# Kernel optimization log

Measured on AMD Instinct MI355X. Metric: run time of the kernel, lower is better.

## Reference

```python
import jax, jax.numpy as jnp
import numpy as np

B, T, S0 = 8, 4, 4096
D_MODEL, H, D, R, RANK = 2048, 16, 128, 64, 512
C = D - R  # content dim = 64


def _rope(x, positions):
    # x: [B, H, T, R]; rotate-half style RoPE as in the torch module
    half = x.shape[-1] // 2
    inv_freq = 1.0 / (10000.0 ** (jnp.arange(half, dtype=jnp.float32) / half))
    freqs = positions.astype(jnp.float32)[:, None] * inv_freq[None, :]  # [T, half]
    cos = jnp.cos(freqs)[None, None].astype(x.dtype)
    sin = jnp.sin(freqs)[None, None].astype(x.dtype)
    x1, x2 = x[..., :half], x[..., half:]
    return jnp.concatenate([x1 * cos - x2 * sin, x1 * sin + x2 * cos], axis=-1)


def setup_inputs() -> dict:
    key = jax.random.key(0)
    ks = jax.random.split(key, 9)
    s = 0.02
    return {
        "x": jax.random.normal(ks[0], (B, T, D_MODEL), jnp.float32),
        "cache_c_kv": jax.random.normal(ks[1], (B, S0, RANK), jnp.float32),
        "cache_k_rope": jax.random.normal(ks[2], (B, S0, H, R), jnp.float32),
        "w_q": jax.random.normal(ks[3], (D_MODEL, H * C), jnp.float32) * s,
        "w_q_rope": jax.random.normal(ks[4], (D_MODEL, H * R), jnp.float32) * s,
        "w_kv_down": jax.random.normal(ks[5], (D_MODEL, RANK), jnp.float32) * s,
        "w_kv_up": jax.random.normal(ks[6], (RANK, H * D), jnp.float32) * s,
        "w_k_rope": jax.random.normal(ks[7], (D_MODEL, H * R), jnp.float32) * s,
        "w_out": jax.random.normal(ks[8], (H * D, D_MODEL), jnp.float32) * s,
    }


def reference(x, cache_c_kv, cache_k_rope, w_q, w_q_rope, w_kv_down, w_kv_up, w_k_rope, w_out):
    cache_len = cache_c_kv.shape[1]
    positions = jnp.arange(cache_len, cache_len + T)

    # queries
    q_content = (x @ w_q).reshape(B, T, H, C).transpose(0, 2, 1, 3)        # [B,H,T,C]
    q_rope = (x @ w_q_rope).reshape(B, T, H, R).transpose(0, 2, 1, 3)      # [B,H,T,R]
    q_rope = _rope(q_rope, positions)
    q = jnp.concatenate([q_content, q_rope], axis=-1)                       # [B,H,T,D]

    # new compressed kv + rope keys, append to cache
    c_kv_new = x @ w_kv_down                                                # [B,T,RANK]
    k_rope_new = (x @ w_k_rope).reshape(B, T, H, R).transpose(0, 2, 1, 3)
    k_rope_new = _rope(k_rope_new, positions).transpose(0, 2, 1, 3)         # [B,T,H,R]
    c_kv = jnp.concatenate([cache_c_kv, c_kv_new], axis=1)                  # [B,S,RANK]
    k_rope = jnp.concatenate([cache_k_rope, k_rope_new], axis=1)            # [B,S,H,R]

    # decompress full cache every step (the expensive MLA pattern)
    S = c_kv.shape[1]
    kv = (c_kv @ w_kv_up).reshape(B, S, H, D)                               # [B,S,H,D]
    k_content = kv[..., :C].transpose(0, 2, 1, 3)                           # [B,H,S,C]
    v = kv.transpose(0, 2, 1, 3)                                            # [B,H,S,D]
    k = jnp.concatenate([k_content, k_rope.transpose(0, 2, 1, 3)], axis=-1) # [B,H,S,D]

    # kv_cache present => is_prefill False => no causal mask (faithful to source)
    scale = 1.0 / jnp.sqrt(jnp.asarray(D, dtype=q.dtype))
    scores = jnp.einsum('bhtd,bhsd->bhts', q, k) * scale
    attn = jax.nn.softmax(scores, axis=-1)
    out = jnp.einsum('bhts,bhsd->bhtd', attn, v)                            # [B,H,T,D]
    out = out.transpose(0, 2, 1, 3).reshape(B, T, H * D)
    return out @ w_out                                                       # [B,T,D_MODEL]
```

## Files before the change

kernel.cpp:

```cpp
#include <hip/hip_runtime.h>
#include <hip/hip_fp16.h>
#include <cmath>

#define BB 8
#define TT 4
#define HH 16
#define DDIM 128
#define RRDIM 64
#define CCDIM 64
#define RANKC 512
#define DMODEL 2048
#define S0C 4096
#define NQ 64
#define HD 2048
#define NACT 3584
#define NSC 65
#define NG 17
#define SPAD 4160
#define SCALE_ATT 0.08838834764831845f

typedef __attribute__((ext_vector_type(8))) short bf16x8;
typedef __attribute__((ext_vector_type(4))) float f32x4;
typedef unsigned short ushortT;

#define AIDX(row, kk) ((row)*132 + (((row)>>2)<<2) + (kk))

static __device__ __forceinline__ unsigned short f2bf(float x) {
  unsigned u = __float_as_uint(x);
  u += 0x7FFFu + ((u >> 16) & 1u);
  return (unsigned short)(u >> 16);
}
static __device__ __forceinline__ unsigned pk2(float a, float b) {
  return (unsigned)f2bf(a) | ((unsigned)f2bf(b) << 16);
}

__global__ __launch_bounds__(256) void k_front(const float* __restrict__ A,
                                               const float* __restrict__ w0,
                                               const float* __restrict__ w1,
                                               const float* __restrict__ w2,
                                               const float* __restrict__ w3,
                                               float* __restrict__ part,
                                               ushortT* __restrict__ ckvB,
                                               ushortT* __restrict__ ckvT,
                                               float* __restrict__ rctab) {
  __shared__ float shf[4352];
  const int tid = threadIdx.x;
  const int bx = blockIdx.x;
  if (bx < 448) {
    const int cb = bx % 28;
    const int k0 = (bx / 28) * 128;
    const float* W; int N, lc0, off;
    if (cb < 8)       { W = w0; N = 1024; lc0 = cb * 128;        off = 0; }
    else if (cb < 16) { W = w1; N = 1024; lc0 = (cb - 8) * 128;  off = 1024; }
    else if (cb < 20) { W = w2; N = 512;  lc0 = (cb - 16) * 128; off = 2048; }
    else              { W = w3; N = 1024; lc0 = (cb - 20) * 128; off = 2560; }
    {
      const int row = tid >> 3;
      const int kseg = (tid & 7) * 16;
      const float4* s4 = reinterpret_cast<const float4*>(A + (size_t)row * DMODEL + k0 + kseg);
      float4 v0 = s4[0], v1 = s4[1], v2 = s4[2], v3 = s4[3];
      *reinterpret_cast<float4*>(&shf[AIDX(row, kseg)])      = v0;
      *reinterpret_cast<float4*>(&shf[AIDX(row, kseg + 4)])  = v1;
      *reinterpret_cast<float4*>(&shf[AIDX(row, kseg + 8)])  = v2;
      *reinterpret_cast<float4*>(&shf[AIDX(row, kseg + 12)]) = v3;
    }
    __syncthreads();
    const int cg = tid & 31;
    const int rg = tid >> 5;
    float acc[4][4];
    #pragma unroll
    for (int r = 0; r < 4; ++r)
      #pragma unroll
      for (int c = 0; c < 4; ++c) acc[r][c] = 0.f;
    #pragma unroll 4
    for (int kk = 0; kk < 128; ++kk) {
      const float4 w4 = *reinterpret_cast<const float4*>(W + (size_t)(k0 + kk) * N + lc0 + cg * 4);
      const float wv[4] = {w4.x, w4.y, w4.z, w4.w};
      #pragma unroll
      for (int r = 0; r < 4; ++r) {
        const float av = shf[AIDX(rg * 4 + r, kk)];
        #pragma unroll
        for (int c = 0; c < 4; ++c) acc[r][c] = fmaf(av, wv[c], acc[r][c]);
      }
    }
    #pragma unroll
    for (int r = 0; r < 4; ++r) {
      float4 o = make_float4(acc[r][0], acc[r][1], acc[r][2], acc[r][3]);
      *reinterpret_cast<float4*>(part + ((size_t)(bx / 28) * 32 + rg * 4 + r) * NACT + off + lc0 + cg * 4) = o;
    }
  } else {
    const int b = bx - 448;
    const uint4 z = make_uint4(0, 0, 0, 0);
    uint4* p = reinterpret_cast<uint4*>(ckvT + ((size_t)(b * NSC + 64) * RANKC) * 64);
    for (int i = tid; i < 4096; i += 256) p[i] = z;
    uint4* q = reinterpret_cast<uint4*>(ckvB + (((size_t)(b * NSC + 64) * 64) + 4) * RANKC);
    for (int i = tid; i < 3840; i += 256) q[i] = z;
    if (bx == 448 && tid < 128) {
      const int t = tid >> 5, j = tid & 31;
      const double fr = (double)(S0C + t) * pow(10000.0, -(double)j / 32.0);
      rctab[t * 32 + j]       = (float)cos(fr);
      rctab[128 + t * 32 + j] = (float)sin(fr);
    }
  }
}

__global__ __launch_bounds__(256) void k_mid(const float* __restrict__ part0,
                                             const float* __restrict__ cache_kr,
                                             const float* __restrict__ wup,
                                             const float* __restrict__ rctab,
                                             const float* __restrict__ cckv,
                                             ushortT* __restrict__ qlat,
                                             ushortT* __restrict__ ckvB,
                                             ushortT* __restrict__ ckvT,
                                             __half* __restrict__ rs) {
  __shared__ float smid[10880];
  const int tid = threadIdx.x;
  const int bx = blockIdx.x;
  if (bx < 1152) {
    const int bh = bx / 9, sy = bx % 9;
    const int b = bh >> 4, h = bh & 15;
    float* raw_q = smid;
    float* raw_k = smid + 256;
    float* qr_l  = smid + 512;
    float* kr_l  = smid + 768;
    {
      const int t = tid >> 6, j = tid & 63;
      const size_t rowoff = (size_t)(b * TT + t) * NACT;
      float sq = 0.f, sk = 0.f;
      #pragma unroll 4
      for (int ks = 0; ks < 16; ++ks) {
        const float* pp = part0 + (size_t)ks * (32 * NACT) + rowoff;
        sq += pp[1024 + h * 64 + j];
        sk += pp[2560 + h * 64 + j];
      }
      raw_q[t * 64 + j] = sq;
      raw_k[t * 64 + j] = sk;
    }
    __syncthreads();
    {
      const int t = tid >> 6, j = tid & 63;
      const int j2 = j & 31;
      const float cs = rctab[t * 32 + j2];
      const float sn = rctab[128 + t * 32 + j2];
      const float qa = raw_q[t * 64 + j], qp = raw_q[t * 64 + (j ^ 32)];
      const float ka = raw_k[t * 64 + j], kp = raw_k[t * 64 + (j ^ 32)];
      float qv, kv;
      if (j < 32) { qv = qa * cs - qp * sn; kv = ka * cs - kp * sn; }
      else        { qv = qp * sn + qa * cs; kv = kp * sn + ka * cs; }
      qr_l[t * 64 + j] = qv * SCALE_ATT;
      kr_l[t * 64 + j] = kv;
    }
    __syncthreads();
    const int ql = tid & 3;
    float4 qf[4][4];
    #pragma unroll
    for (int t = 0; t < 4; ++t)
      #pragma unroll
      for (int u = 0; u < 4; ++u)
        qf[t][u] = *reinterpret_cast<const float4*>(&qr_l[t * 64 + ql * 16 + u * 4]);
    const int s0 = sy * 512;
    #pragma unroll 2
    for (int pass = 0; pass < 8; ++pass) {
      const int s = s0 + pass * 64 + (tid >> 2);
      if (s < 4100) {
        float p[4] = {0.f, 0.f, 0.f, 0.f};
        const float* krow = (s < S0C)
            ? cache_kr + (((size_t)b * S0C + s) * HH + h) * RRDIM
            : &kr_l[(s - S0C) * 64];
        #pragma unroll
        for (int u = 0; u < 4; ++u) {
          const float4 kv = *reinterpret_cast<const float4*>(krow + ql * 16 + u * 4);
          #pragma unroll
          for (int t = 0; t < 4; ++t)
            p[t] += kv.x * qf[t][u].x + kv.y * qf[t][u].y
                  + kv.z * qf[t][u].z + kv.w * qf[t][u].w;
        }
        #pragma unroll
        for (int t = 0; t < 4; ++t) {
          p[t] += __shfl_xor(p[t], 1, 4);
          p[t] += __shfl_xor(p[t], 2, 4);
        }
        rs[((size_t)bh * 4 + ql) * SPAD + s] = __float2half(p[ql]);
      }
    }
  } else if (bx < 1216) {
    const int lx = bx - 1152;
    const int h = lx & 15;
    const int r0 = (lx >> 4) * 128;
    float* wt  = smid;
    float* a_s = smid + 8448;
    {
      const int r = tid >> 1;
      const int cseg = (tid & 1) * 32;
      const float* src = wup + (size_t)(r0 + r) * HD + h * DDIM + cseg;
      #pragma unroll
      for (int u = 0; u < 8; ++u) {
        const float4 v = *reinterpret_cast<const float4*>(src + u * 4);
        wt[(cseg + u * 4 + 0) * 132 + r] = v.x;
        wt[(cseg + u * 4 + 1) * 132 + r] = v.y;
        wt[(cseg + u * 4 + 2) * 132 + r] = v.z;
        wt[(cseg + u * 4 + 3) * 132 + r] = v.w;
      }
    }
    {
      const int bt = tid >> 3;
      const int c8 = (tid & 7) * 8;
      float v[8] = {0.f,0.f,0.f,0.f,0.f,0.f,0.f,0.f};
      #pragma unroll 4
      for (int ks = 0; ks < 16; ++ks) {
        const float4* pp = reinterpret_cast<const float4*>(
            part0 + (size_t)ks * (32 * NACT) + (size_t)bt * NACT + h * CCDIM + c8);
        const float4 x0 = pp[0], x1 = pp[1];
        v[0]+=x0.x; v[1]+=x0.y; v[2]+=x0.z; v[3]+=x0.w;
        v[4]+=x1.x; v[5]+=x1.y; v[6]+=x1.z; v[7]+=x1.w;
      }
      #pragma unroll
      for (int u = 0; u < 8; ++u) a_s[bt * 68 + c8 + u] = v[u];
    }
    __syncthreads();
    const int r = tid & 127;
    const int bth = tid >> 7;
    float acc[16];
    #pragma unroll
    for (int i = 0; i < 16; ++i) acc[i] = 0.f;
    #pragma unroll 8
    for (int c = 0; c < 64; ++c) {
      const float wv = wt[c * 132 + r];
      #pragma unroll
      for (int i = 0; i < 16; ++i)
        acc[i] = fmaf(a_s[(bth * 16 + i) * 68 + c], wv, acc[i]);
    }
    #pragma unroll
    for (int i = 0; i < 16; ++i) {
      const int bt = bth * 16 + i;
      const int b = bt >> 2, t = bt & 3;
      qlat[((size_t)(b * NQ) + h * TT + t) * RANKC + r0 + r] = f2bf(acc[i]);
    }
  } else if (bx < 1280) {
    const int g = (bx - 1216) * 256 + tid;
    const int r = g & 511;
    const int bt = g >> 9;
    const int b = bt >> 2, t = bt & 3;
    float s = 0.f;
    #pragma unroll 4
    for (int ks = 0; ks < 16; ++ks)
      s += part0[(size_t)ks * (32 * NACT) + (size_t)bt * NACT + 2048 + r];
    const ushortT bv = f2bf(s);
    ckvB[(((size_t)(b * NSC + 64) * 64) + t) * RANKC + r] = bv;
    ckvT[(((size_t)(b * NSC + 64) * RANKC) + r) * 64 + t] = bv;
  } else {
    ushortT* tlds = reinterpret_cast<ushortT*>(smid);
    const int idx = bx - 1280;
    const int b = idx >> 6, c = idx & 63;
    const float* src = cckv + ((size_t)b * S0C + c * 64) * RANKC;
    ushortT* dstB = ckvB + ((size_t)(b * NSC + c) * 64) * RANKC;
    ushortT* dstT = ckvT + ((size_t)(b * NSC + c) * RANKC) * 64;
    const int s = tid >> 2, rq = tid & 3;
    const int rloc = tid >> 1, shalf = (tid & 1) * 32;
    for (int slab = 0; slab < 4; ++slab) {
      const int r0 = slab * 128;
      unsigned pk_arr[16];
      #pragma unroll
      for (int i = 0; i < 8; ++i) {
        const float4 v = *reinterpret_cast<const float4*>(src + (size_t)s * RANKC + r0 + rq * 32 + i * 4);
        pk_arr[2 * i]     = pk2(v.x, v.y);
        pk_arr[2 * i + 1] = pk2(v.z, v.w);
        *reinterpret_cast<uint2*>(&tlds[s * 136 + rq * 32 + i * 4]) =
            make_uint2(pk_arr[2 * i], pk_arr[2 * i + 1]);
      }
      {
        uint4* db = reinterpret_cast<uint4*>(dstB + (size_t)s * RANKC + r0 + rq * 32);
        db[0] = make_uint4(pk_arr[0], pk_arr[1], pk_arr[2], pk_arr[3]);
        db[1] = make_uint4(pk_arr[4], pk_arr[5], pk_arr[6], pk_arr[7]);
        db[2] = make_uint4(pk_arr[8], pk_arr[9], pk_arr[10], pk_arr[11]);
        db[3] = make_uint4(pk_arr[12], pk_arr[13], pk_arr[14], pk_arr[15]);
      }
      __syncthreads();
      unsigned pkv[16];
      #pragma unroll
      for (int k = 0; k < 16; ++k) {
        const unsigned t0 = tlds[(shalf + 2 * k)     * 136 + rloc];
        const unsigned t1 = tlds[(shalf + 2 * k + 1) * 136 + rloc];
        pkv[k] = t0 | (t1 << 16);
      }
      uint4* d = reinterpret_cast<uint4*>(dstT + ((size_t)(r0 + rloc)) * 64 + shalf);
      d[0] = make_uint4(pkv[0], pkv[1], pkv[2], pkv[3]);
      d[1] = make_uint4(pkv[4], pkv[5], pkv[6], pkv[7]);
      d[2] = make_uint4(pkv[8], pkv[9], pkv[10], pkv[11]);
      d[3] = make_uint4(pkv[12], pkv[13], pkv[14], pkv[15]);
      __syncthreads();
    }
  }
}

__global__ __launch_bounds__(256) void k_score(
    const ushortT* __restrict__ ckvB, const ushortT* __restrict__ qlat,
    const __half* __restrict__ rs, float* __restrict__ ml,
    ushortT* __restrict__ Pg) {
  __shared__ ushortT PL[64 * 72];
  const int tid = threadIdx.x;
  const int wv = tid >> 6;
  const int lane = tid & 63;
  const int lm = lane & 15, lg = lane >> 4;
  const int b = blockIdx.x, chunk = blockIdx.y;
  const int qbase = wv * 16;
  const int scnt = (chunk < 64) ? 64 : TT;
  const ushortT* bsrc = ckvB + ((size_t)(b * NSC + chunk) * 64) * RANKC;

  const ushortT* qrow = qlat + ((size_t)b * NQ + qbase + lm) * RANKC + lg * 8;
  bf16x8 qa[16];
  #pragma unroll
  for (int ks = 0; ks < 16; ++ks)
    qa[ks] = *reinterpret_cast<const bf16x8*>(qrow + ks * 32);

  f32x4 acc[4];
  #pragma unroll
  for (int st = 0; st < 4; ++st) acc[st] = (f32x4){0.f, 0.f, 0.f, 0.f};
  #pragma unroll
  for (int ks = 0; ks < 16; ++ks) {
    #pragma unroll
    for (int st = 0; st < 4; ++st) {
      const bf16x8 bf = *reinterpret_cast<const bf16x8*>(
          bsrc + (size_t)(st * 16 + lm) * RANKC + ks * 32 + lg * 8);
      acc[st] = __builtin_amdgcn_mfma_f32_16x16x32_bf16(qa[ks], bf, acc[st], 0, 0, 0);
    }
  }

  #pragma unroll
  for (int reg = 0; reg < 4; ++reg) {
    const int qi = qbase + lg * 4 + reg;
    const __half* rp = rs + (((size_t)(b * HH) + (qi >> 2)) * TT + (qi & 3)) * SPAD + chunk * 64;
    float vvv[4];
    float mx = -1e30f;
    #pragma unroll
    for (int st = 0; st < 4; ++st) {
      const int sl = st * 16 + lm;
      const float val = (sl < scnt)
          ? fmaf(acc[st][reg], SCALE_ATT, __half2float(rp[sl]))
          : -1e30f;
      vvv[st] = val;
      mx = fmaxf(mx, val);
    }
    #pragma unroll
    for (int off = 1; off < 16; off <<= 1) mx = fmaxf(mx, __shfl_xor(mx, off, 16));
    float sum = 0.f;
    #pragma unroll
    for (int st = 0; st < 4; ++st) {
      const float p = __expf(vvv[st] - mx);
      vvv[st] = p;
      sum += p;
    }
    #pragma unroll
    for (int off = 1; off < 16; off <<= 1) sum += __shfl_xor(sum, off, 16);
    #pragma unroll
    for (int st = 0; st < 4; ++st)
      PL[(qbase + lg * 4 + reg) * 72 + st * 16 + lm] = f2bf(vvv[st]);
    if (lm == 0) {
      const size_t mb = (((size_t)b * NSC + chunk) * NQ + qi) * 2;
      ml[mb] = mx; ml[mb + 1] = sum;
    }
  }
  __syncthreads();
  {
    const int row = tid >> 2, seg = (tid & 3) * 16;
    const uint4* sp = reinterpret_cast<const uint4*>(&PL[row * 72 + seg]);
    uint4* dp = reinterpret_cast<uint4*>(
        Pg + ((size_t)(b * NSC + chunk) * NQ + row) * 64 + seg);
    dp[0] = sp[0]; dp[1] = sp[1];
  }
}

__global__ __launch_bounds__(256) void k_pv(
    const ushortT* __restrict__ ckvT, const ushortT* __restrict__ Pg,
    const float* __restrict__ ml, float* __restrict__ olat,
    float* __restrict__ mlg) {
  const int tid = threadIdx.x;
  const int wv = tid >> 6;
  const int lane = tid & 63;
  const int lm = lane & 15, lg = lane >> 4;
  const int b = blockIdx.x, g = blockIdx.y, rg = blockIdx.z;
  const int qbase = wv * 16;
  const int nc = (g < 16) ? 4 : 1;
  const int c0 = (g < 16) ? g * 4 : 64;

  float m_cl = -1e30f, l_cl = 0.f;
  if (lg < nc) {
    const size_t mb = (((size_t)b * NSC + c0 + lg) * NQ + qbase + lm) * 2;
    m_cl = ml[mb]; l_cl = ml[mb + 1];
  }
  float mg = fmaxf(m_cl, __shfl_xor(m_cl, 16));
  mg = fmaxf(mg, __shfl_xor(mg, 32));
  const float wgt = (lg < nc) ? __expf(m_cl - mg) : 0.f;
  float la = l_cl * wgt;
  la += __shfl_xor(la, 16);
  la += __shfl_xor(la, 32);
  if (rg == 0 && lg == 0) {
    const size_t gb = (((size_t)b * NG + g) * NQ + qbase + lm) * 2;
    mlg[gb] = mg; mlg[gb + 1] = la;
  }
  float wf[4][4];
  #pragma unroll
  for (int c = 0; c < 4; ++c)
    #pragma unroll
    for (int reg = 0; reg < 4; ++reg)
      wf[c][reg] = __shfl(wgt, c * 16 + lg * 4 + reg);

  f32x4 OACC[8];
  #pragma unroll
  for (int nt = 0; nt < 8; ++nt) OACC[nt] = (f32x4){0.f, 0.f, 0.f, 0.f};

  for (int c = 0; c < nc; ++c) {
    const ushortT* pb = Pg + ((size_t)(b * NSC + c0 + c) * NQ + qbase + lm) * 64 + lg * 8;
    const bf16x8 pa0 = *reinterpret_cast<const bf16x8*>(pb);
    const bf16x8 pa1 = *reinterpret_cast<const bf16x8*>(pb + 32);
    const ushortT* vb = ckvT + (((size_t)(b * NSC + c0 + c) * RANKC) + rg * 128 + lm) * 64 + lg * 8;
    f32x4 a2[8];
    #pragma unroll
    for (int nt = 0; nt < 8; ++nt) a2[nt] = (f32x4){0.f, 0.f, 0.f, 0.f};
    #pragma unroll
    for (int nt = 0; nt < 8; ++nt) {
      const bf16x8 b0 = *reinterpret_cast<const bf16x8*>(vb + (size_t)nt * 16 * 64);
      const bf16x8 b1 = *reinterpret_cast<const bf16x8*>(vb + (size_t)nt * 16 * 64 + 32);
      a2[nt] = __builtin_amdgcn_mfma_f32_16x16x32_bf16(pa0, b0, a2[nt], 0, 0, 0);
      a2[nt] = __builtin_amdgcn_mfma_f32_16x16x32_bf16(pa1, b1, a2[nt], 0, 0, 0);
    }
    const f32x4 wv4 = {wf[c][0], wf[c][1], wf[c][2], wf[c][3]};
    #pragma unroll
    for (int nt = 0; nt < 8; ++nt) OACC[nt] += wv4 * a2[nt];
  }

  const size_t obase = ((size_t)(b * NG + g) * NQ) * RANKC;
  #pragma unroll
  for (int nt = 0; nt < 8; ++nt)
    #pragma unroll
    for (int reg = 0; reg < 4; ++reg)
      olat[obase + (size_t)(qbase + lg * 4 + reg) * RANKC + rg * 128 + nt * 16 + lm] = OACC[nt][reg];
}

__global__ __launch_bounds__(512) void k_combF(const float* __restrict__ mlg,
                                               const float* __restrict__ olat,
                                               const float* __restrict__ wup,
                                               float* __restrict__ ohead,
                                               float* __restrict__ out) {
  __shared__ float wrow[4][20];
  __shared__ float att_lds[4][516];
  __shared__ float red[4][4][32][4];
  const int h = blockIdx.x, b = blockIdx.y;
  const int tid = threadIdx.x;
  {
    const int t = tid >> 7, col = tid & 127;
    out[(size_t)(b * TT + t) * HD + h * DDIM + col] = 0.f;
  }
  const int wave = tid >> 6;
  const int i = wave >> 1;
  const int rhalf = wave & 1;
  const int rl = tid & 63;
  const int qi = h * TT + i;
  float m1 = -1e30f, l1 = 0.f;
  if (rl < NG) {
    const size_t base = (((size_t)b * NG + rl) * NQ + qi) * 2;
    m1 = mlg[base]; l1 = mlg[base + 1];
  }
  float M = m1;
  #pragma unroll
  for (int off = 1; off < 64; off <<= 1) M = fmaxf(M, __shfl_xor(M, off));
  float L = (rl < NG) ? l1 * __expf(m1 - M) : 0.f;
  #pragma unroll
  for (int off = 1; off < 64; off <<= 1) L += __shfl_xor(L, off);
  const float invL = 1.0f / L;
  if (rl < NG) wrow[i][rl] = __expf(m1 - M) * invL;
  __syncthreads();
  const int r0 = rhalf * 256 + rl * 4;
  {
    float o0 = 0.f, o1 = 0.f, o2 = 0.f, o3 = 0.f;
    for (int c = 0; c < NG; ++c) {
      const float w = wrow[i][c];
      const float4 v = *reinterpret_cast<const float4*>(
          olat + (((size_t)b * NG + c) * NQ + qi) * RANKC + r0);
      o0 = fmaf(v.x, w, o0); o1 = fmaf(v.y, w, o1);
      o2 = fmaf(v.z, w, o2); o3 = fmaf(v.w, w, o3);
    }
    *reinterpret_cast<float4*>(&att_lds[i][r0]) = make_float4(o0, o1, o2, o3);
  }
  __syncthreads();
  const int t = tid >> 7;
  const int rq = (tid >> 5) & 3;
  const int c4 = tid & 31;
  const float* wb = wup + (size_t)h * DDIM + c4 * 4;
  float a0 = 0.f, a1 = 0.f, a2 = 0.f, a3 = 0.f;
  const int rbeg = rq * 128;
  #pragma unroll 4
  for (int rr = 0; rr < 128; ++rr) {
    const int r = rbeg + rr;
    const float4 w4 = *reinterpret_cast<const float4*>(wb + (size_t)r * HD);
    const float a = att_lds[t][r];
    a0 = fmaf(a, w4.x, a0); a1 = fmaf(a, w4.y, a1);
    a2 = fmaf(a, w4.z, a2); a3 = fmaf(a, w4.w, a3);
  }
  *reinterpret_cast<float4*>(&red[rq][t][c4][0]) = make_float4(a0, a1, a2, a3);
  __syncthreads();
  if (tid < 128) {
    const int t2 = tid >> 5, c42 = tid & 31;
    float4 s = make_float4(0.f, 0.f, 0.f, 0.f);
    #pragma unroll
    for (int q = 0; q < 4; ++q) {
      const float4 v = *reinterpret_cast<const float4*>(&red[q][t2][c42][0]);
      s.x += v.x; s.y += v.y; s.z += v.z; s.w += v.w;
    }
    *reinterpret_cast<float4*>(&ohead[(size_t)(b * TT + t2) * HD + h * DDIM + c42 * 4]) = s;
  }
}

__global__ __launch_bounds__(256) void k_projA(const float* __restrict__ A,
                                               const float* __restrict__ W,
                                               float* __restrict__ out) {
  __shared__ float a_lds[4352];
  const int tid = threadIdx.x;
  const int c0 = blockIdx.x * 128;
  const int k0 = blockIdx.y * 128;
  {
    const int row = tid >> 3;
    const int kseg = (tid & 7) * 16;
    const float4* s4 = reinterpret_cast<const float4*>(A + (size_t)row * DMODEL + k0 + kseg);
    float4 v0 = s4[0], v1 = s4[1], v2 = s4[2], v3 = s4[3];
    *reinterpret_cast<float4*>(&a_lds[AIDX(row, kseg)])      = v0;
    *reinterpret_cast<float4*>(&a_lds[AIDX(row, kseg + 4)])  = v1;
    *reinterpret_cast<float4*>(&a_lds[AIDX(row, kseg + 8)])  = v2;
    *reinterpret_cast<float4*>(&a_lds[AIDX(row, kseg + 12)]) = v3;
  }
  __syncthreads();
  const int cg = tid & 31;
  const int rg = tid >> 5;
  float acc[4][4];
  #pragma unroll
  for (int r = 0; r < 4; ++r)
    #pragma unroll
    for (int c = 0; c < 4; ++c) acc[r][c] = 0.f;
  #pragma unroll 4
  for (int kk = 0; kk < 128; ++kk) {
    const float4 w4 = *reinterpret_cast<const float4*>(W + (size_t)(k0 + kk) * HD + c0 + cg * 4);
    const float wv[4] = {w4.x, w4.y, w4.z, w4.w};
    #pragma unroll
    for (int r = 0; r < 4; ++r) {
      const float av = a_lds[AIDX(rg * 4 + r, kk)];
      #pragma unroll
      for (int c = 0; c < 4; ++c) acc[r][c] = fmaf(av, wv[c], acc[r][c]);
    }
  }
  #pragma unroll
  for (int r = 0; r < 4; ++r)
    #pragma unroll
    for (int c = 0; c < 4; ++c)
      unsafeAtomicAdd(&out[(size_t)(rg * 4 + r) * HD + c0 + cg * 4 + c], acc[r][c]);
}

extern "C" void kernel_launch(void* const* d_in, const int* in_sizes, int n_in,
                              void* d_out, int out_size, void* d_ws, size_t ws_size,
                              hipStream_t stream) {
  const float* x     = (const float*)d_in[0];
  const float* cckv  = (const float*)d_in[1];
  const float* ckr   = (const float*)d_in[2];
  const float* w_q   = (const float*)d_in[3];
  const float* w_qr  = (const float*)d_in[4];
  const float* w_kvd = (const float*)d_in[5];
  const float* w_kvu = (const float*)d_in[6];
  const float* w_kr  = (const float*)d_in[7];
  const float* w_out = (const float*)d_in[8];
  float* out = (float*)d_out;
  float* ws = (float*)d_ws;

  size_t off = 0;
  ushortT* qlat   = (ushortT*)(ws + off); off += 131072;
  float* mlb      = ws + off; off += (size_t)BB * NSC * NQ * 2;
  float* mlgb     = ws + off; off += (size_t)BB * NG * NQ * 2;
  float* ohead    = ws + off; off += 65536;
  float* rctab    = ws + off; off += 256;
  __half* rsb     = (__half*)(ws + off); off += 1064960;
  ushortT* ckvB   = (ushortT*)(ws + off); off += 8519680;
  ushortT* ckvT   = (ushortT*)(ws + off); off += 8519680;
  ushortT* Pgb    = (ushortT*)(ws + off); off += 1064960;
  float* regB  = ws + off;
  float* part0 = regB;
  float* olat  = regB;

  k_front<<<dim3(456), 256, 0, stream>>>(x, w_q, w_qr, w_kvd, w_kr, part0, ckvB, ckvT, rctab);
  k_mid<<<dim3(1792), 256, 0, stream>>>(part0, ckr, w_kvu, rctab, cckv, qlat, ckvB, ckvT, rsb);
  k_score<<<dim3(BB, NSC), 256, 0, stream>>>(ckvB, qlat, rsb, mlb, Pgb);
  k_pv<<<dim3(BB, NG, 4), 256, 0, stream>>>(ckvT, Pgb, mlb, olat, mlgb);
  k_combF<<<dim3(16, 8), 512, 0, stream>>>(mlgb, olat, w_kvu, ohead, out);
  k_projA<<<dim3(16, 16), 256, 0, stream>>>(ohead, w_out, out);
}
```

Before: 219.2 us.

## Move cache bf16 conversion into front kernel and shrink mid-kernel LDS

Moves the bf16 conversion and transpose of the compressed KV cache from k_mid into k_front, so it runs alongside the projection GEMM blocks and no longer shares k_mid's launch. The q-latent absorption path in k_mid now keeps its w_kv_up row in registers instead of staging a transposed tile in shared memory. That cuts k_mid's LDS from about 43KB to about 8.7KB, which should raise occupancy for its many score blocks. The trade-off is a more register-heavy absorption loop with uncoalesced-per-thread row loads, plus a longer first kernel.

```diff
diff --git a/kernel.cpp b/kernel.cpp
--- a/kernel.cpp
+++ b/kernel.cpp
@@ -39,6 +39,7 @@
                                                const float* __restrict__ w1,
                                                const float* __restrict__ w2,
                                                const float* __restrict__ w3,
+                                               const float* __restrict__ cckv,
                                                float* __restrict__ part,
                                                ushortT* __restrict__ ckvB,
                                                ushortT* __restrict__ ckvT,
@@ -88,14 +89,56 @@
       float4 o = make_float4(acc[r][0], acc[r][1], acc[r][2], acc[r][3]);
       *reinterpret_cast<float4*>(part + ((size_t)(bx / 28) * 32 + rg * 4 + r) * NACT + off + lc0 + cg * 4) = o;
     }
+  } else if (bx < 960) {
+    ushortT* tlds = reinterpret_cast<ushortT*>(shf);
+    const int idx = bx - 448;
+    const int b = idx >> 6, c = idx & 63;
+    const float* src = cckv + ((size_t)b * S0C + c * 64) * RANKC;
+    ushortT* dstB = ckvB + ((size_t)(b * NSC + c) * 64) * RANKC;
+    ushortT* dstT = ckvT + ((size_t)(b * NSC + c) * RANKC) * 64;
+    const int s = tid >> 2, rq = tid & 3;
+    const int rloc = tid >> 1, shalf = (tid & 1) * 32;
+    for (int slab = 0; slab < 4; ++slab) {
+      const int r0 = slab * 128;
+      unsigned pk_arr[16];
+      #pragma unroll
+      for (int i = 0; i < 8; ++i) {
+        const float4 v = *reinterpret_cast<const float4*>(src + (size_t)s * RANKC + r0 + rq * 32 + i * 4);
+        pk_arr[2 * i]     = pk2(v.x, v.y);
+        pk_arr[2 * i + 1] = pk2(v.z, v.w);
+        *reinterpret_cast<uint2*>(&tlds[s * 136 + rq * 32 + i * 4]) =
+            make_uint2(pk_arr[2 * i], pk_arr[2 * i + 1]);
+      }
+      {
+        uint4* db = reinterpret_cast<uint4*>(dstB + (size_t)s * RANKC + r0 + rq * 32);
+        db[0] = make_uint4(pk_arr[0], pk_arr[1], pk_arr[2], pk_arr[3]);
+        db[1] = make_uint4(pk_arr[4], pk_arr[5], pk_arr[6], pk_arr[7]);
+        db[2] = make_uint4(pk_arr[8], pk_arr[9], pk_arr[10], pk_arr[11]);
+        db[3] = make_uint4(pk_arr[12], pk_arr[13], pk_arr[14], pk_arr[15]);
+      }
+      __syncthreads();
+      unsigned pkv[16];
+      #pragma unroll
+      for (int k = 0; k < 16; ++k) {
+        const unsigned t0 = tlds[(shalf + 2 * k)     * 136 + rloc];
+        const unsigned t1 = tlds[(shalf + 2 * k + 1) * 136 + rloc];
+        pkv[k] = t0 | (t1 << 16);
+      }
+      uint4* d = reinterpret_cast<uint4*>(dstT + ((size_t)(r0 + rloc)) * 64 + shalf);
+      d[0] = make_uint4(pkv[0], pkv[1], pkv[2], pkv[3]);
+      d[1] = make_uint4(pkv[4], pkv[5], pkv[6], pkv[7]);
+      d[2] = make_uint4(pkv[8], pkv[9], pkv[10], pkv[11]);
+      d[3] = make_uint4(pkv[12], pkv[13], pkv[14], pkv[15]);
+      __syncthreads();
+    }
   } else {
-    const int b = bx - 448;
+    const int b = bx - 960;
     const uint4 z = make_uint4(0, 0, 0, 0);
     uint4* p = reinterpret_cast<uint4*>(ckvT + ((size_t)(b * NSC + 64) * RANKC) * 64);
     for (int i = tid; i < 4096; i += 256) p[i] = z;
     uint4* q = reinterpret_cast<uint4*>(ckvB + (((size_t)(b * NSC + 64) * 64) + 4) * RANKC);
     for (int i = tid; i < 3840; i += 256) q[i] = z;
-    if (bx == 448 && tid < 128) {
+    if (bx == 960 && tid < 128) {
       const int t = tid >> 5, j = tid & 31;
       const double fr = (double)(S0C + t) * pow(10000.0, -(double)j / 32.0);
       rctab[t * 32 + j]       = (float)cos(fr);
@@ -108,12 +151,11 @@
                                              const float* __restrict__ cache_kr,
                                              const float* __restrict__ wup,
                                              const float* __restrict__ rctab,
-                                             const float* __restrict__ cckv,
                                              ushortT* __restrict__ qlat,
                                              ushortT* __restrict__ ckvB,
                                              ushortT* __restrict__ ckvT,
                                              __half* __restrict__ rs) {
-  __shared__ float smid[10880];
+  __shared__ float smid[2176];
   const int tid = threadIdx.x;
   const int bx = blockIdx.x;
   if (bx < 1152) {
@@ -187,21 +229,7 @@
     const int lx = bx - 1152;
     const int h = lx & 15;
     const int r0 = (lx >> 4) * 128;
-    float* wt  = smid;
-    float* a_s = smid + 8448;
-    {
-      const int r = tid >> 1;
-      const int cseg = (tid & 1) * 32;
-      const float* src = wup + (size_t)(r0 + r) * HD + h * DDIM + cseg;
-      #pragma unroll
-      for (int u = 0; u < 8; ++u) {
-        const float4 v = *reinterpret_cast<const float4*>(src + u * 4);
-        wt[(cseg + u * 4 + 0) * 132 + r] = v.x;
-        wt[(cseg + u * 4 + 1) * 132 + r] = v.y;
-        wt[(cseg + u * 4 + 2) * 132 + r] = v.z;
-        wt[(cseg + u * 4 + 3) * 132 + r] = v.w;
-      }
-    }
+    float* a_s = smid;
     {
       const int bt = tid >> 3;
       const int c8 = (tid & 7) * 8;
@@ -220,15 +248,24 @@
     __syncthreads();
     const int r = tid & 127;
     const int bth = tid >> 7;
+    const float* wrow = wup + (size_t)(r0 + r) * HD + h * DDIM;
+    float4 wreg[16];
+    #pragma unroll
+    for (int u = 0; u < 16; ++u)
+      wreg[u] = *reinterpret_cast<const float4*>(wrow + u * 4);
     float acc[16];
     #pragma unroll
     for (int i = 0; i < 16; ++i) acc[i] = 0.f;
-    #pragma unroll 8
-    for (int c = 0; c < 64; ++c) {
-      const float wv = wt[c * 132 + r];
-      #pragma unroll
-      for (int i = 0; i < 16; ++i)
-        acc[i] = fmaf(a_s[(bth * 16 + i) * 68 + c], wv, acc[i]);
+    #pragma unroll
+    for (int u = 0; u < 16; ++u) {
+      #pragma unroll
+      for (int i = 0; i < 16; ++i) {
+        const float4 av = *reinterpret_cast<const float4*>(&a_s[(bth * 16 + i) * 68 + u * 4]);
+        acc[i] = fmaf(av.x, wreg[u].x, acc[i]);
+        acc[i] = fmaf(av.y, wreg[u].y, acc[i]);
+        acc[i] = fmaf(av.z, wreg[u].z, acc[i]);
+        acc[i] = fmaf(av.w, wreg[u].w, acc[i]);
+      }
     }
     #pragma unroll
     for (int i = 0; i < 16; ++i) {
@@ -236,7 +273,7 @@
       const int b = bt >> 2, t = bt & 3;
       qlat[((size_t)(b * NQ) + h * TT + t) * RANKC + r0 + r] = f2bf(acc[i]);
     }
-  } else if (bx < 1280) {
+  } else {
     const int g = (bx - 1216) * 256 + tid;
     const int r = g & 511;
     const int bt = g >> 9;
@@ -248,48 +285,6 @@
     const ushortT bv = f2bf(s);
     ckvB[(((size_t)(b * NSC + 64) * 64) + t) * RANKC + r] = bv;
     ckvT[(((size_t)(b * NSC + 64) * RANKC) + r) * 64 + t] = bv;
-  } else {
-    ushortT* tlds = reinterpret_cast<ushortT*>(smid);
-    const int idx = bx - 1280;
-    const int b = idx >> 6, c = idx & 63;
-    const float* src = cckv + ((size_t)b * S0C + c * 64) * RANKC;
-    ushortT* dstB = ckvB + ((size_t)(b * NSC + c) * 64) * RANKC;
-    ushortT* dstT = ckvT + ((size_t)(b * NSC + c) * RANKC) * 64;
-    const int s = tid >> 2, rq = tid & 3;
-    const int rloc = tid >> 1, shalf = (tid & 1) * 32;
-    for (int slab = 0; slab < 4; ++slab) {
-      const int r0 = slab * 128;
-      unsigned pk_arr[16];
-      #pragma unroll
-      for (int i = 0; i < 8; ++i) {
-        const float4 v = *reinterpret_cast<const float4*>(src + (size_t)s * RANKC + r0 + rq * 32 + i * 4);
-        pk_arr[2 * i]     = pk2(v.x, v.y);
-        pk_arr[2 * i + 1] = pk2(v.z, v.w);
-        *reinterpret_cast<uint2*>(&tlds[s * 136 + rq * 32 + i * 4]) =
-            make_uint2(pk_arr[2 * i], pk_arr[2 * i + 1]);
-      }
-      {
-        uint4* db = reinterpret_cast<uint4*>(dstB + (size_t)s * RANKC + r0 + rq * 32);
-        db[0] = make_uint4(pk_arr[0], pk_arr[1], pk_arr[2], pk_arr[3]);
-        db[1] = make_uint4(pk_arr[4], pk_arr[5], pk_arr[6], pk_arr[7]);
-        db[2] = make_uint4(pk_arr[8], pk_arr[9], pk_arr[10], pk_arr[11]);
-        db[3] = make_uint4(pk_arr[12], pk_arr[13], pk_arr[14], pk_arr[15]);
-      }
-      __syncthreads();
-      unsigned pkv[16];
-      #pragma unroll
-      for (int k = 0; k < 16; ++k) {
-        const unsigned t0 = tlds[(shalf + 2 * k)     * 136 + rloc];
-        const unsigned t1 = tlds[(shalf + 2 * k + 1) * 136 + rloc];
-        pkv[k] = t0 | (t1 << 16);
-      }
-      uint4* d = reinterpret_cast<uint4*>(dstT + ((size_t)(r0 + rloc)) * 64 + shalf);
-      d[0] = make_uint4(pkv[0], pkv[1], pkv[2], pkv[3]);
-      d[1] = make_uint4(pkv[4], pkv[5], pkv[6], pkv[7]);
-      d[2] = make_uint4(pkv[8], pkv[9], pkv[10], pkv[11]);
-      d[3] = make_uint4(pkv[12], pkv[13], pkv[14], pkv[15]);
-      __syncthreads();
-    }
   }
 }
 
@@ -583,8 +578,8 @@
   float* part0 = regB;
   float* olat  = regB;
 
-  k_front<<<dim3(456), 256, 0, stream>>>(x, w_q, w_qr, w_kvd, w_kr, part0, ckvB, ckvT, rctab);
-  k_mid<<<dim3(1792), 256, 0, stream>>>(part0, ckr, w_kvu, rctab, cckv, qlat, ckvB, ckvT, rsb);
+  k_front<<<dim3(968), 256, 0, stream>>>(x, w_q, w_qr, w_kvd, w_kr, cckv, part0, ckvB, ckvT, rctab);
+  k_mid<<<dim3(1280), 256, 0, stream>>>(part0, ckr, w_kvu, rctab, qlat, ckvB, ckvT, rsb);
   k_score<<<dim3(BB, NSC), 256, 0, stream>>>(ckvB, qlat, rsb, mlb, Pgb);
   k_pv<<<dim3(BB, NG, 4), 256, 0, stream>>>(ckvT, Pgb, mlb, olat, mlgb);
   k_combF<<<dim3(16, 8), 512, 0, stream>>>(mlgb, olat, w_kvu, ohead, out);
```

After: 210.1 us. 1.04x faster.
